# Kernel tuning notes

Hardware: AMD Instinct MI355X
Metric: run time of the kernel (lower is better)

The kernel has to match this reference:

```python
import jax, jax.numpy as jnp
import numpy as np

N_ASSETS = 512
WINDOW = 256
BATCH = 32
THRESHOLDS = (0.3, 0.5, 0.7)
N_SQUARINGS = 9  # ceil(log2(N_ASSETS)); reachability converges after log2(n) squarings


def setup_inputs() -> dict:
    key = jax.random.key(0)
    returns = jax.random.normal(key, (BATCH, WINDOW, N_ASSETS), dtype=jnp.float32)
    return {"returns": returns}


def _betti_features(corr):
    """corr: (B, N, N). Returns (B, 2*len(THRESHOLDS)) Betti features."""
    B, N, _ = corr.shape
    eye = jnp.eye(N, dtype=jnp.float32)
    idx = jnp.arange(N)
    feats = []
    for t in THRESHOLDS:
        # adjacency with zeroed diagonal (matches np.fill_diagonal(adj, 0))
        adj = (jnp.abs(corr) > t).astype(jnp.float32) * (1.0 - eye)
        # transitive closure via repeated boolean squaring of (A | I)
        R = jnp.minimum(adj + eye, 1.0)
        for _ in range(N_SQUARINGS):
            R = (jnp.einsum('bij,bjk->bik', R, R) > 0).astype(jnp.float32)
        # component representative of node i = smallest reachable index;
        # number of components = count of self-representatives
        comp_rep = jnp.argmax(R, axis=-1)              # first 1 along row = min index
        components = jnp.sum(comp_rep == idx[None, :], axis=-1).astype(jnp.float32)
        edges = jnp.sum(adj, axis=(-1, -2)) / 2.0
        betti0 = components
        betti1 = jnp.maximum(0.0, edges - N + components)
        feats.append(betti0 / N)
        feats.append(betti1 / N)
    return jnp.stack(feats, axis=-1)  # (B, 2*n_thresholds), order [t0_b0, t0_b1, t1_b0, ...]


def reference(returns) -> jnp.ndarray:
    B, W, N = returns.shape
    ret_centered = returns - returns.mean(axis=1, keepdims=True)
    # torch .std() is unbiased (ddof=1)
    std = jnp.std(ret_centered, axis=1, keepdims=True, ddof=1) + 1e-8
    ret_normalized = ret_centered / std
    corr = jnp.einsum('bwi,bwj->bij', ret_normalized, ret_normalized) / W
    return _betti_features(corr)
```

## Files before the change

### kernel.cpp

```cpp
#include <hip/hip_runtime.h>
#include <hip/hip_bf16.h>
#include <stdint.h>

#define NASSETS 512
#define WINDOW  256
#define NBATCH  32
#define NWORDS  16
#define BM 128
#define BN 128

typedef __attribute__((ext_vector_type(4))) float floatx4;
typedef __attribute__((ext_vector_type(4))) int   intx4;
typedef __attribute__((ext_vector_type(2))) long  longx2;

__device__ __forceinline__ unsigned int f2e4m3_manual(float x) {
    union { float f; unsigned u; } c; c.f = x;
    unsigned s = (c.u >> 24) & 0x80u;
    unsigned a = c.u & 0x7FFFFFFFu;
    float af = fabsf(x);
    unsigned code;
    if (af >= 448.f) code = 0x7Eu;
    else if (af < 0.015625f) {
        code = (unsigned)(int)rintf(af * 512.f);
    } else {
        unsigned E = a >> 23;
        unsigned base = ((E - 120u) << 3) | ((a >> 20) & 7u);
        unsigned rem = a & 0xFFFFFu;
        if (rem > 0x80000u || (rem == 0x80000u && (base & 1u))) base++;
        if (base > 0x7Eu) base = 0x7Eu;
        code = base;
    }
    return s | code;
}

__device__ __forceinline__ int pack4fp8(float f0, float f1, float f2, float f3) {
#if defined(__has_builtin) && __has_builtin(__builtin_amdgcn_cvt_pk_fp8_f32)
    int v = 0;
    v = __builtin_amdgcn_cvt_pk_fp8_f32(f0, f1, v, false);
    v = __builtin_amdgcn_cvt_pk_fp8_f32(f2, f3, v, true);
    return v;
#else
    return (int)(f2e4m3_manual(f0) | (f2e4m3_manual(f1) << 8) |
                 (f2e4m3_manual(f2) << 16) | (f2e4m3_manual(f3) << 24));
#endif
}

__device__ __forceinline__ void gload16(const void* gp, void* lp) {
    __builtin_amdgcn_global_load_lds(
        (const __attribute__((address_space(1))) void*)(uintptr_t)gp,
        (__attribute__((address_space(3))) void*)(unsigned int)(uintptr_t)lp,
        16, 0, 0);
}

__global__ __launch_bounds__(1024)
void normalize_kernel(const float* __restrict__ ret, char* __restrict__ Xt) {
    __shared__ float sred[1024];
    __shared__ float ssred[1024];
    __shared__ float smean[64];
    __shared__ float sinv[64];
    __shared__ __align__(16) char tile[64 * 256];

    const int t  = threadIdx.x;
    const int a  = t & 63;
    const int wc = t >> 6;
    const int g  = blockIdx.x;
    const int b  = blockIdx.y;
    const int n0 = g * 64;

    const float* base = ret + (size_t)b * WINDOW * NASSETS + n0 + a;

    float x[16];
    float s1 = 0.f, s2 = 0.f;
#pragma unroll
    for (int k = 0; k < 16; ++k) {
        x[k] = base[(size_t)(wc * 16 + k) * NASSETS];
        s1 += x[k];
        s2 += x[k] * x[k];
    }
    sred[wc * 64 + a]  = s1;
    ssred[wc * 64 + a] = s2;
    __syncthreads();

    if (t < 64) {
        float S = 0.f, S2 = 0.f;
#pragma unroll
        for (int c = 0; c < 16; ++c) { S += sred[c * 64 + t]; S2 += ssred[c * 64 + t]; }
        float mean = S / (float)WINDOW;
        float var  = (S2 - (float)WINDOW * mean * mean) / (float)(WINDOW - 1);
        if (var < 0.f) var = 0.f;
        float stdv = sqrtf(var) + 1e-8f;
        smean[t] = mean;
        sinv[t]  = 1.0f / stdv;
    }
    __syncthreads();

    const float mn = smean[a];
    const float iv = sinv[a];

    int pk[4];
#pragma unroll
    for (int j = 0; j < 4; ++j)
        pk[j] = pack4fp8((x[4*j+0] - mn) * iv, (x[4*j+1] - mn) * iv,
                         (x[4*j+2] - mn) * iv, (x[4*j+3] - mn) * iv);

    char* rowp = tile + a * 256;
    const int s     = wc >> 2;
    const int h8    = (wc & 2) ? 8 : 0;
    const int qbase = (wc & 1) * 2;
#pragma unroll
    for (int q = 0; q < 2; ++q) {
        unsigned long long piece = (unsigned)pk[2*q] |
                                   ((unsigned long long)(unsigned)pk[2*q+1] << 32);
        int L = s * 4 + qbase + q;
        *(unsigned long long*)(rowp + ((L ^ (a & 15)) * 16) + h8) = piece;
    }
    __syncthreads();

    char* orow = Xt + ((size_t)b * NASSETS + n0) * WINDOW;
    {
        int r  = t >> 4;
        int sl = t & 15;
        intx4 v = *(const intx4*)(tile + r * 256 + ((sl ^ (r & 15)) * 16));
        *(intx4*)(orow + r * WINDOW + sl * 16) = v;
    }
}

__global__ __launch_bounds__(256)
void corr_adj_kernel(const char* __restrict__ Xt, unsigned int* __restrict__ adj) {
    __shared__ __align__(16) char lsA[BM * 64];
    __shared__ __align__(16) char lsB[BN * 64];

    const int t    = threadIdx.x;
    const int lane = t & 63;
    const int wave = t >> 6;
    const int wi   = wave >> 1, wj = wave & 1;
    const int b  = blockIdx.z;
    const int i0 = blockIdx.y * BM;
    const int j0 = blockIdx.x * BN;

    const char* base = Xt + (size_t)b * NASSETS * WINDOW;

    const int m  = lane & 15;
    const int kq = lane >> 4;
    const int srowAdd  = lane >> 2;
    const int gslotOff = ((lane & 3) ^ ((lane >> 2) & 3)) * 16;

    floatx4 acc[4][4] = {};

    for (int k0 = 0; k0 < WINDOW; k0 += 64) {
        __syncthreads();
#pragma unroll
        for (int c = 0; c < 2; ++c) {
            int r0 = (wave * 2 + c) * 16;
            const char* gA = base + (size_t)(i0 + r0 + srowAdd) * WINDOW + k0 + gslotOff;
            const char* gB = base + (size_t)(j0 + r0 + srowAdd) * WINDOW + k0 + gslotOff;
            gload16(gA, (char*)lsA + r0 * 64);
            gload16(gB, (char*)lsB + r0 * 64);
        }
        __syncthreads();

        longx2 af[4], bf[4];
#pragma unroll
        for (int mi = 0; mi < 4; ++mi) {
            int r = wi * 64 + mi * 16 + m;
            af[mi] = *(const longx2*)(lsA + r * 64 + ((kq ^ (r & 3)) * 16));
        }
#pragma unroll
        for (int nj = 0; nj < 4; ++nj) {
            int r = wj * 64 + nj * 16 + m;
            bf[nj] = *(const longx2*)(lsB + r * 64 + ((kq ^ (r & 3)) * 16));
        }
#pragma unroll
        for (int mi = 0; mi < 4; ++mi)
#pragma unroll
            for (int nj = 0; nj < 4; ++nj) {
                acc[mi][nj] = __builtin_amdgcn_mfma_f32_16x16x32_fp8_fp8(
                    af[mi].x, bf[nj].x, acc[mi][nj], 0, 0, 0);
                acc[mi][nj] = __builtin_amdgcn_mfma_f32_16x16x32_fp8_fp8(
                    af[mi].y, bf[nj].y, acc[mi][nj], 0, 0, 0);
            }
    }

    const float T[3] = {0.3f * (float)WINDOW, 0.5f * (float)WINDOW, 0.7f * (float)WINDOW};
    unsigned int wout[3][2] = {{0u,0u},{0u,0u},{0u,0u}};
    const int qp = (lane >> 2) & 3;
#pragma unroll
    for (int mi = 0; mi < 4; ++mi) {
#pragma unroll
        for (int r = 0; r < 4; ++r) {
            bool act = ((lane >> 4) == mi) && ((lane & 3) == r);
#pragma unroll
            for (int th = 0; th < 3; ++th) {
                unsigned long long b0 = __ballot(fabsf(acc[mi][0][r]) > T[th]);
                unsigned long long b1 = __ballot(fabsf(acc[mi][1][r]) > T[th]);
                unsigned long long b2 = __ballot(fabsf(acc[mi][2][r]) > T[th]);
                unsigned long long b3 = __ballot(fabsf(acc[mi][3][r]) > T[th]);
                if (act) {
                    wout[th][0] = ((unsigned)(b0 >> (qp * 16)) & 0xFFFFu)
                                | (((unsigned)(b1 >> (qp * 16)) & 0xFFFFu) << 16);
                    wout[th][1] = ((unsigned)(b2 >> (qp * 16)) & 0xFFFFu)
                                | (((unsigned)(b3 >> (qp * 16)) & 0xFFFFu) << 16);
                }
            }
        }
    }

    const int grow    = i0 + wi * 64 + lane;
    const int colbase = j0 + wj * 64;
    unsigned int dd = (unsigned int)(grow - colbase);
    if (dd < 64u) {
        unsigned int m0 = (dd < 32u) ? ~(1u << dd) : 0xFFFFFFFFu;
        unsigned int m1 = (dd >= 32u) ? ~(1u << (dd - 32u)) : 0xFFFFFFFFu;
#pragma unroll
        for (int th = 0; th < 3; ++th) { wout[th][0] &= m0; wout[th][1] &= m1; }
    }
    const int wb = colbase >> 5;
    const size_t stride_t = (size_t)NBATCH * NASSETS * NWORDS;
    size_t rb = ((size_t)b * NASSETS + grow) * NWORDS + wb;
#pragma unroll
    for (int th = 0; th < 3; ++th) {
        adj[rb + th * stride_t]     = wout[th][0];
        adj[rb + th * stride_t + 1] = wout[th][1];
    }
}

__global__ __launch_bounds__(512)
void betti_kernel(const unsigned int* __restrict__ adj, float* __restrict__ out) {
    __shared__ int lab[NASSETS];
    __shared__ int changed;
    __shared__ int red[8];

    int th = blockIdx.x;
    int b  = blockIdx.y;
    int i  = threadIdx.x;
    int lane = i & 63, wv = i >> 6;

    const unsigned int* rowp =
        adj + (((size_t)th * NBATCH + b) * NASSETS + i) * NWORDS;
    unsigned int row[NWORDS];
    int deg = 0;
#pragma unroll
    for (int w = 0; w < NWORDS; ++w) {
        row[w] = rowp[w];
        deg += __popc(row[w]);
    }

    int v = deg;
#pragma unroll
    for (int off = 32; off > 0; off >>= 1) v += __shfl_down(v, off);
    if (lane == 0) red[wv] = v;
    lab[i] = i;
    __syncthreads();
    int total_deg = 0;
    if (i == 0)
        for (int k = 0; k < 8; ++k) total_deg += red[k];

    for (;;) {
        __syncthreads();
        if (i == 0) changed = 0;
        __syncthreads();
        int mlab = lab[i];
#pragma unroll
        for (int w = 0; w < NWORDS; ++w) {
            unsigned int bits = row[w];
            int basej = w * 32;
            while (bits) {
                int j = basej + __builtin_ctz(bits);
                bits &= bits - 1;
                int lj = lab[j];
                if (lj < mlab) mlab = lj;
            }
        }
        int lm = lab[mlab];
        if (lm < mlab) mlab = lm;
        __syncthreads();
        if (mlab < lab[i]) { lab[i] = mlab; changed = 1; }
        __syncthreads();
        if (!changed) break;
    }

    int isrep = (lab[i] == i) ? 1 : 0;
#pragma unroll
    for (int off = 32; off > 0; off >>= 1) isrep += __shfl_down(isrep, off);
    if (lane == 0) red[wv] = isrep;
    __syncthreads();
    if (i == 0) {
        int comps = 0;
        for (int k = 0; k < 8; ++k) comps += red[k];
        float compf = (float)comps;
        float edges = (float)total_deg * 0.5f;
        out[b * 6 + th * 2 + 0] = compf / (float)NASSETS;
        out[b * 6 + th * 2 + 1] = fmaxf(0.0f, edges - (float)NASSETS + compf) / (float)NASSETS;
    }
}

extern "C" void kernel_launch(void* const* d_in, const int* in_sizes, int n_in,
                              void* d_out, int out_size, void* d_ws, size_t ws_size,
                              hipStream_t stream) {
    const float* ret = (const float*)d_in[0];
    float* out = (float*)d_out;
    char* ws = (char*)d_ws;

    char* Xt = ws;
    unsigned int* adj =
        (unsigned int*)(ws + (size_t)NBATCH * NASSETS * WINDOW);

    dim3 g1(NASSETS / 64, NBATCH);
    normalize_kernel<<<g1, 1024, 0, stream>>>(ret, Xt);

    dim3 g2(NASSETS / BN, NASSETS / BM, NBATCH);
    corr_adj_kernel<<<g2, 256, 0, stream>>>(Xt, adj);

    dim3 g3(3, NBATCH);
    betti_kernel<<<g3, 512, 0, stream>>>(adj, out);
}
```

Before: 77.86 us.

## Stage full K panel in LDS for corr and vectorize normalize loads

```diff
diff --git a/kernel.cpp b/kernel.cpp
--- a/kernel.cpp
+++ b/kernel.cpp
@@ -52,39 +52,50 @@
         16, 0, 0);
 }
 
-__global__ __launch_bounds__(1024)
+__global__ __launch_bounds__(512)
 void normalize_kernel(const float* __restrict__ ret, char* __restrict__ Xt) {
-    __shared__ float sred[1024];
-    __shared__ float ssred[1024];
-    __shared__ float smean[64];
-    __shared__ float sinv[64];
-    __shared__ __align__(16) char tile[64 * 256];
+    __shared__ __align__(16) char raw[32768];
+    __shared__ float sred[512];
+    __shared__ float ssred[512];
+    __shared__ float smean[32];
+    __shared__ float sinv[32];
 
     const int t  = threadIdx.x;
-    const int a  = t & 63;
-    const int wc = t >> 6;
     const int g  = blockIdx.x;
     const int b  = blockIdx.y;
-    const int n0 = g * 64;
-
-    const float* base = ret + (size_t)b * WINDOW * NASSETS + n0 + a;
-
+    const int n0 = g * 32;
+
+    const float* gbase = ret + (size_t)b * WINDOW * NASSETS + n0;
+    float* rawf = (float*)raw;
+
+#pragma unroll
+    for (int i = 0; i < 4; ++i) {
+        int f  = i * 512 + t;
+        int w  = f >> 3;
+        int nq = f & 7;
+        floatx4 v = *(const floatx4*)(gbase + (size_t)w * NASSETS + nq * 4);
+        *(floatx4*)(raw + w * 128 + nq * 16) = v;
+    }
+    __syncthreads();
+
+    const int a  = t & 31;
+    const int wc = t >> 5;
     float x[16];
     float s1 = 0.f, s2 = 0.f;
 #pragma unroll
     for (int k = 0; k < 16; ++k) {
-        x[k] = base[(size_t)(wc * 16 + k) * NASSETS];
+        x[k] = rawf[(wc * 16 + k) * 32 + a];
         s1 += x[k];
         s2 += x[k] * x[k];
     }
-    sred[wc * 64 + a]  = s1;
-    ssred[wc * 64 + a] = s2;
-    __syncthreads();
-
-    if (t < 64) {
+    sred[wc * 32 + a]  = s1;
+    ssred[wc * 32 + a] = s2;
+    __syncthreads();
+
+    if (t < 32) {
         float S = 0.f, S2 = 0.f;
 #pragma unroll
-        for (int c = 0; c < 16; ++c) { S += sred[c * 64 + t]; S2 += ssred[c * 64 + t]; }
+        for (int c = 0; c < 16; ++c) { S += sred[c * 32 + t]; S2 += ssred[c * 32 + t]; }
         float mean = S / (float)WINDOW;
         float var  = (S2 - (float)WINDOW * mean * mean) / (float)(WINDOW - 1);
         if (var < 0.f) var = 0.f;
@@ -103,7 +114,7 @@
         pk[j] = pack4fp8((x[4*j+0] - mn) * iv, (x[4*j+1] - mn) * iv,
                          (x[4*j+2] - mn) * iv, (x[4*j+3] - mn) * iv);
 
-    char* rowp = tile + a * 256;
+    char* rowp = raw + a * 256;
     const int s     = wc >> 2;
     const int h8    = (wc & 2) ? 8 : 0;
     const int qbase = (wc & 1) * 2;
@@ -120,15 +131,15 @@
     {
         int r  = t >> 4;
         int sl = t & 15;
-        intx4 v = *(const intx4*)(tile + r * 256 + ((sl ^ (r & 15)) * 16));
+        intx4 v = *(const intx4*)(raw + r * 256 + ((sl ^ (r & 15)) * 16));
         *(intx4*)(orow + r * WINDOW + sl * 16) = v;
     }
 }
 
 __global__ __launch_bounds__(256)
 void corr_adj_kernel(const char* __restrict__ Xt, unsigned int* __restrict__ adj) {
-    __shared__ __align__(16) char lsA[BM * 64];
-    __shared__ __align__(16) char lsB[BN * 64];
+    __shared__ __align__(16) char lsA[BM * 256];
+    __shared__ __align__(16) char lsB[BN * 256];
 
     const int t    = threadIdx.x;
     const int lane = t & 63;
@@ -142,33 +153,36 @@
 
     const int m  = lane & 15;
     const int kq = lane >> 4;
-    const int srowAdd  = lane >> 2;
-    const int gslotOff = ((lane & 3) ^ ((lane >> 2) & 3)) * 16;
+
+    const int rl = lane >> 4;
+    const int pl = lane & 15;
+
+#pragma unroll
+    for (int c = 0; c < 8; ++c) {
+        int r0 = wave * 32 + c * 4;
+        int rr = (r0 & 15) + rl;
+        int gs = (pl ^ rr) * 16;
+        const char* gA = base + (size_t)(i0 + r0 + rl) * WINDOW + gs;
+        const char* gB = base + (size_t)(j0 + r0 + rl) * WINDOW + gs;
+        gload16(gA, (char*)lsA + r0 * 256);
+        gload16(gB, (char*)lsB + r0 * 256);
+    }
+    __syncthreads();
 
     floatx4 acc[4][4] = {};
 
-    for (int k0 = 0; k0 < WINDOW; k0 += 64) {
-        __syncthreads();
-#pragma unroll
-        for (int c = 0; c < 2; ++c) {
-            int r0 = (wave * 2 + c) * 16;
-            const char* gA = base + (size_t)(i0 + r0 + srowAdd) * WINDOW + k0 + gslotOff;
-            const char* gB = base + (size_t)(j0 + r0 + srowAdd) * WINDOW + k0 + gslotOff;
-            gload16(gA, (char*)lsA + r0 * 64);
-            gload16(gB, (char*)lsB + r0 * 64);
-        }
-        __syncthreads();
-
+#pragma unroll
+    for (int s = 0; s < 4; ++s) {
         longx2 af[4], bf[4];
 #pragma unroll
         for (int mi = 0; mi < 4; ++mi) {
             int r = wi * 64 + mi * 16 + m;
-            af[mi] = *(const longx2*)(lsA + r * 64 + ((kq ^ (r & 3)) * 16));
+            af[mi] = *(const longx2*)(lsA + r * 256 + (((s * 4 + kq) ^ (r & 15)) * 16));
         }
 #pragma unroll
         for (int nj = 0; nj < 4; ++nj) {
             int r = wj * 64 + nj * 16 + m;
-            bf[nj] = *(const longx2*)(lsB + r * 64 + ((kq ^ (r & 3)) * 16));
+            bf[nj] = *(const longx2*)(lsB + r * 256 + (((s * 4 + kq) ^ (r & 15)) * 16));
         }
 #pragma unroll
         for (int mi = 0; mi < 4; ++mi)
@@ -305,8 +319,8 @@
     unsigned int* adj =
         (unsigned int*)(ws + (size_t)NBATCH * NASSETS * WINDOW);
 
-    dim3 g1(NASSETS / 64, NBATCH);
-    normalize_kernel<<<g1, 1024, 0, stream>>>(ret, Xt);
+    dim3 g1(NASSETS / 32, NBATCH);
+    normalize_kernel<<<g1, 512, 0, stream>>>(ret, Xt);
 
     dim3 g2(NASSETS / BN, NASSETS / BM, NBATCH);
     corr_adj_kernel<<<g2, 256, 0, stream>>>(Xt, adj);
```

New measurement: 77.88 us. About the same (+0.0%).
